# Optimization experiments

Hardware: AMD Instinct MI355X
Metric: run time of the kernel (lower is better)

## Reference

```python
import jax, jax.numpy as jnp
import numpy as np

P = 9    # patch_size (number of shifts per axis)
DP = 1   # dilation_patch (pixel step per shift)


def setup_inputs() -> dict:
    key = jax.random.key(0)
    k1, k2 = jax.random.split(key)
    input1 = jax.random.normal(k1, (4, 256, 96, 128), dtype=jnp.float32)
    input2 = jax.random.normal(k2, (4, 256, 96, 128), dtype=jnp.float32)
    return {"input1": input1, "input2": input2}


def _correlation(input1, input2):
    # Faithful to iter_spatial_correlation_sample with kernel_size=1, stride=1,
    # padding=0, dilation=1: offsets are integer pixel shifts, and bilinear
    # grid_sample (align_corners=True, zeros outside) at integer coordinates is
    # exactly a zero-padded integer shift of input2.
    b, c, h, w = input2.shape
    off = DP * ((P - 1) // 2)  # center offset in pixels
    pad2 = jnp.pad(input2, ((0, 0), (0, 0), (off, off), (off, off)))
    rows = []
    for i in range(P):          # small fixed loop over patch offsets (81 total)
        cols = []
        for j in range(P):
            # window = input2 shifted by (dy, dx) = (i*DP - off, j*DP - off)
            win = jax.lax.dynamic_slice(pad2, (0, 0, i * DP, j * DP), (b, c, h, w))
            cols.append(jnp.einsum('bchw,bchw->bhw', input1, win))
        rows.append(jnp.stack(cols, axis=1))  # [b, P, h, w]
    return jnp.stack(rows, axis=1)            # [b, P, P, h, w]


def reference(input1, input2):
    return _correlation(input1, input2)
```

## Files before the change

### kernel.cpp

```cpp
#include <hip/hip_runtime.h>

#define BB 4
#define CC 256
#define HH 96
#define WW 128
#define PP 9
#define OFF 4
#define CCH 16
#define NPAIR (CCH / 2)
#define NCH (CC / CCH)
#define TPB 288
#define TW 72
#define XCOLS 64

typedef _Float16 h2 __attribute__((ext_vector_type(2)));

__device__ __forceinline__ h2 u2h(unsigned u) { union { unsigned u; h2 h; } x; x.u = u; return x.h; }

#if __has_builtin(__builtin_amdgcn_fdot2)
__device__ __forceinline__ float dot2(h2 a, h2 b, float c) { return __builtin_amdgcn_fdot2(a, b, c, false); }
#else
__device__ __forceinline__ float dot2(h2 a, h2 b, float c) { return c + (float)a[0] * (float)b[0] + (float)a[1] * (float)b[1]; }
#endif

__device__ __forceinline__ unsigned pk(float a, float b) {
#if __has_builtin(__builtin_amdgcn_cvt_pkrtz)
  auto r = __builtin_amdgcn_cvt_pkrtz(a, b);
  unsigned u; __builtin_memcpy(&u, &r, 4); return u;
#else
  h2 h; h[0] = (_Float16)a; h[1] = (_Float16)b;
  unsigned u; __builtin_memcpy(&u, &h, 4); return u;
#endif
}

__global__ __launch_bounds__(TPB, 4) void corr_kernel(const float* __restrict__ in1,
                                                      const float* __restrict__ in2,
                                                      float* __restrict__ out) {
  __shared__ unsigned s2[NPAIR][PP][TW];
  __shared__ unsigned s1[NPAIR][XCOLS];

  const int bx = blockIdx.x;
  const int xcd = bx & 7;
  const int slot = bx >> 3;
  const int xh = slot & 1;
  const int s3 = slot >> 1;
  const int b = s3 / 12;
  const int h = xcd * 12 + (s3 % 12);
  const int xbase = xh * XCOLS;

  const int tid = threadIdx.x;
  const int dy = tid >> 5;
  const int pxg = tid & 31;
  const int L0 = pxg << 1;

  const int sp = tid / 36;
  const int sc2 = tid - sp * 36;
  const int sL = sc2 << 1;
  const int sgx = xbase - OFF + sL;
  const bool colv = (sgx >= 0) && (sgx < WW);
  const int rlo = (h >= OFF) ? 0 : (OFF - h);
  const int rhi = (PP < HH + OFF - h) ? PP : (HH + OFF - h);

  const int plane = HH * WW;
  const long base_b = (long)b * CC * plane;

  const float* p2a = in2 + base_b + (long)(2 * sp) * plane + (long)(h - OFF) * WW + sgx;
  const float* p2b = p2a + plane;
  const int i1p = tid >> 5, i1c = tid & 31;
  const float* p1a = in1 + base_b + (long)(2 * i1p) * plane + h * WW + xbase + (i1c << 1);
  const float* p1b = p1a + plane;

  for (int i = tid; i < NPAIR * PP * TW; i += TPB) ((unsigned*)s2)[i] = 0u;

  float acc[2][PP];
#pragma unroll
  for (int px = 0; px < 2; ++px)
#pragma unroll
    for (int dx = 0; dx < PP; ++dx) acc[px][dx] = 0.f;

  float2 fa[PP], fb[PP], ga, gb;

  if (colv) {
#pragma unroll
    for (int r = 0; r < PP; ++r)
      if (r >= rlo && r < rhi) {
        fa[r] = *(const float2*)(p2a + r * WW);
        fb[r] = *(const float2*)(p2b + r * WW);
      }
  }
  if (tid < NPAIR * 32) { ga = *(const float2*)p1a; gb = *(const float2*)p1b; }
  __syncthreads();

#pragma unroll 1
  for (int c = 0; c < NCH; ++c) {
    if (colv) {
#pragma unroll
      for (int r = 0; r < PP; ++r)
        if (r >= rlo && r < rhi)
          *(uint2*)&s2[sp][r][sL] = make_uint2(pk(fa[r].x, fb[r].x), pk(fa[r].y, fb[r].y));
    }
    if (tid < NPAIR * 32)
      *(uint2*)&s1[i1p][i1c << 1] = make_uint2(pk(ga.x, gb.x), pk(ga.y, gb.y));
    __syncthreads();

    if (c + 1 < NCH) {
      const long adv = (long)(c + 1) * CCH * plane;
      if (colv) {
#pragma unroll
        for (int r = 0; r < PP; ++r)
          if (r >= rlo && r < rhi) {
            fa[r] = *(const float2*)(p2a + adv + r * WW);
            fb[r] = *(const float2*)(p2b + adv + r * WW);
          }
      }
      if (tid < NPAIR * 32) { ga = *(const float2*)(p1a + adv); gb = *(const float2*)(p1b + adv); }
    }

#pragma unroll
    for (int p = 0; p < NPAIR; ++p) {
      unsigned q[2], w[10];
      *(uint2*)q = *(const uint2*)&s1[p][L0];
#pragma unroll
      for (int i = 0; i < 5; ++i)
        *(uint2*)&w[2 * i] = *(const uint2*)&s2[p][dy][L0 + 2 * i];
#pragma unroll
      for (int px = 0; px < 2; ++px)
#pragma unroll
        for (int dx = 0; dx < PP; ++dx)
          acc[px][dx] = dot2(u2h(w[px + dx]), u2h(q[px]), acc[px][dx]);
    }
    __syncthreads();
  }

  const int gx0 = xbase + L0;
  float* ob = out + ((long)(b * PP + dy) * PP) * plane + h * WW + gx0;
#pragma unroll
  for (int dx = 0; dx < PP; ++dx)
    *(float2*)(ob + (long)dx * plane) = make_float2(acc[0][dx], acc[1][dx]);
}

extern "C" void kernel_launch(void* const* d_in, const int* in_sizes, int n_in,
                              void* d_out, int out_size, void* d_ws, size_t ws_size,
                              hipStream_t stream) {
  const float* in1 = (const float*)d_in[0];
  const float* in2 = (const float*)d_in[1];
  float* out = (float*)d_out;
  corr_kernel<<<dim3(BB * HH * 2), dim3(TPB), 0, stream>>>(in1, in2, out);
}
```

Measured before the change: 160.3 us.

## Double-buffer LDS tiles and use one LDS-only barrier per channel chunk

Shared-memory tiles become double-buffered, so the next chunk's fp16-packed data is written into the alternate buffer right after computing on the current one. This removes one of the two barriers per channel chunk. A custom barrier waits only on LDS counters (lgkmcnt) so global prefetches two chunks ahead can stay in flight across it. The cost is twice the LDS footprint, which may lower occupancy, plus more live prefetch registers.

```diff
diff --git a/kernel.cpp b/kernel.cpp
--- a/kernel.cpp
+++ b/kernel.cpp
@@ -33,11 +33,19 @@
 #endif
 }
 
+__device__ __forceinline__ void bar_lgkm() {
+  __builtin_amdgcn_sched_barrier(0);
+  asm volatile("s_waitcnt lgkmcnt(0)" ::: "memory");
+  __builtin_amdgcn_s_barrier();
+  asm volatile("" ::: "memory");
+  __builtin_amdgcn_sched_barrier(0);
+}
+
 __global__ __launch_bounds__(TPB, 4) void corr_kernel(const float* __restrict__ in1,
                                                       const float* __restrict__ in2,
                                                       float* __restrict__ out) {
-  __shared__ unsigned s2[NPAIR][PP][TW];
-  __shared__ unsigned s1[NPAIR][XCOLS];
+  __shared__ unsigned s2[2][NPAIR][PP][TW];
+  __shared__ unsigned s1[2][NPAIR][XCOLS];
 
   const int bx = blockIdx.x;
   const int xcd = bx & 7;
@@ -70,7 +78,7 @@
   const float* p1a = in1 + base_b + (long)(2 * i1p) * plane + h * WW + xbase + (i1c << 1);
   const float* p1b = p1a + plane;
 
-  for (int i = tid; i < NPAIR * PP * TW; i += TPB) ((unsigned*)s2)[i] = 0u;
+  for (int i = tid; i < 2 * NPAIR * PP * TW; i += TPB) ((unsigned*)s2)[i] = 0u;
 
   float acc[2][PP];
 #pragma unroll
@@ -80,56 +88,64 @@
 
   float2 fa[PP], fb[PP], ga, gb;
 
-  if (colv) {
+  auto PREFETCH = [&](int c) {
+    const long adv = (long)c * CCH * plane;
+    if (colv) {
 #pragma unroll
-    for (int r = 0; r < PP; ++r)
-      if (r >= rlo && r < rhi) {
-        fa[r] = *(const float2*)(p2a + r * WW);
-        fb[r] = *(const float2*)(p2b + r * WW);
-      }
-  }
-  if (tid < NPAIR * 32) { ga = *(const float2*)p1a; gb = *(const float2*)p1b; }
-  __syncthreads();
+      for (int r = 0; r < PP; ++r)
+        if (r >= rlo && r < rhi) {
+          fa[r] = *(const float2*)(p2a + adv + r * WW);
+          fb[r] = *(const float2*)(p2b + adv + r * WW);
+        }
+    }
+    if (tid < NPAIR * 32) {
+      ga = *(const float2*)(p1a + adv);
+      gb = *(const float2*)(p1b + adv);
+    }
+  };
 
-#pragma unroll 1
-  for (int c = 0; c < NCH; ++c) {
+  auto STORE = [&](int buf) {
     if (colv) {
 #pragma unroll
       for (int r = 0; r < PP; ++r)
         if (r >= rlo && r < rhi)
-          *(uint2*)&s2[sp][r][sL] = make_uint2(pk(fa[r].x, fb[r].x), pk(fa[r].y, fb[r].y));
+          *(uint2*)&s2[buf][sp][r][sL] = make_uint2(pk(fa[r].x, fb[r].x), pk(fa[r].y, fb[r].y));
     }
     if (tid < NPAIR * 32)
-      *(uint2*)&s1[i1p][i1c << 1] = make_uint2(pk(ga.x, gb.x), pk(ga.y, gb.y));
-    __syncthreads();
+      *(uint2*)&s1[buf][i1p][i1c << 1] = make_uint2(pk(ga.x, gb.x), pk(ga.y, gb.y));
+  };
 
-    if (c + 1 < NCH) {
-      const long adv = (long)(c + 1) * CCH * plane;
-      if (colv) {
-#pragma unroll
-        for (int r = 0; r < PP; ++r)
-          if (r >= rlo && r < rhi) {
-            fa[r] = *(const float2*)(p2a + adv + r * WW);
-            fb[r] = *(const float2*)(p2b + adv + r * WW);
-          }
-      }
-      if (tid < NPAIR * 32) { ga = *(const float2*)(p1a + adv); gb = *(const float2*)(p1b + adv); }
-    }
+  PREFETCH(0);
+  bar_lgkm();
+
+  STORE(0);
+  PREFETCH(1);
+  bar_lgkm();
+
+#pragma unroll 1
+  for (int c = 0; c < NCH; ++c) {
+    const unsigned (*S2)[PP][TW] = s2[c & 1];
+    const unsigned (*S1)[XCOLS] = s1[c & 1];
 
 #pragma unroll
     for (int p = 0; p < NPAIR; ++p) {
       unsigned q[2], w[10];
-      *(uint2*)q = *(const uint2*)&s1[p][L0];
+      *(uint2*)q = *(const uint2*)&S1[p][L0];
 #pragma unroll
       for (int i = 0; i < 5; ++i)
-        *(uint2*)&w[2 * i] = *(const uint2*)&s2[p][dy][L0 + 2 * i];
+        *(uint2*)&w[2 * i] = *(const uint2*)&S2[p][dy][L0 + 2 * i];
 #pragma unroll
       for (int px = 0; px < 2; ++px)
 #pragma unroll
         for (int dx = 0; dx < PP; ++dx)
           acc[px][dx] = dot2(u2h(w[px + dx]), u2h(q[px]), acc[px][dx]);
     }
-    __syncthreads();
+
+    if (c + 1 < NCH) {
+      STORE((c + 1) & 1);
+      if (c + 2 < NCH) PREFETCH(c + 2);
+      bar_lgkm();
+    }
   }
 
   const int gx0 = xbase + L0;
```

Result: slower. 519.0 us (+223.7%).

## Compute correlation with MFMA 16x16x32 f16 tiles over 3-row bands

Applied to the files above, without the earlier changes.

Replaces the per-thread fdot2 accumulation with MFMA matrix instructions. Each block handles a 3-row by 32-pixel tile and computes a 32x32 pixel-pair Gram block per dy, then extracts the 9 diagonals through shared memory. The staging and tiling are restructured around this: channels are packed in chunks of 32, the in2 rows are shared across three output rows, and the grid is reshaped to 512 blocks. About two thirds of the MFMA work is off-diagonal and gets discarded. The epilogue adds extra syncs and strided scalar stores, and the register prefetch of the next chunk is dropped.

```diff
diff --git a/kernel.cpp b/kernel.cpp
--- a/kernel.cpp
+++ b/kernel.cpp
@@ -6,137 +6,142 @@
 #define WW 128
 #define PP 9
 #define OFF 4
-#define CCH 16
-#define NPAIR (CCH / 2)
-#define NCH (CC / CCH)
-#define TPB 288
-#define TW 72
-#define XCOLS 64
+#define PLANE (HH * WW)
 
-typedef _Float16 h2 __attribute__((ext_vector_type(2)));
+#define HB 3
+#define RN (HB + 8)
+#define PX 32
+#define SW 48
+#define PAD 20
+#define KCH 32
+#define NCHK (CC / KCH)
+#define TPB 384
+#define DPAD 36
 
-__device__ __forceinline__ h2 u2h(unsigned u) { union { unsigned u; h2 h; } x; x.u = u; return x.h; }
+typedef _Float16 f16x8 __attribute__((ext_vector_type(8)));
+typedef float fx4 __attribute__((ext_vector_type(4)));
 
-#if __has_builtin(__builtin_amdgcn_fdot2)
-__device__ __forceinline__ float dot2(h2 a, h2 b, float c) { return __builtin_amdgcn_fdot2(a, b, c, false); }
-#else
-__device__ __forceinline__ float dot2(h2 a, h2 b, float c) { return c + (float)a[0] * (float)b[0] + (float)a[1] * (float)b[1]; }
-#endif
+union U16 { uint4 u; f16x8 h; };
 
 __device__ __forceinline__ unsigned pk(float a, float b) {
 #if __has_builtin(__builtin_amdgcn_cvt_pkrtz)
   auto r = __builtin_amdgcn_cvt_pkrtz(a, b);
   unsigned u; __builtin_memcpy(&u, &r, 4); return u;
 #else
-  h2 h; h[0] = (_Float16)a; h[1] = (_Float16)b;
-  unsigned u; __builtin_memcpy(&u, &h, 4); return u;
+  _Float16 h0 = (_Float16)a, h1 = (_Float16)b;
+  unsigned u = 0; __builtin_memcpy(&u, &h0, 2); unsigned v = 0; __builtin_memcpy(&v, &h1, 2);
+  return u | (v << 16);
 #endif
 }
 
-__global__ __launch_bounds__(TPB, 4) void corr_kernel(const float* __restrict__ in1,
+__global__ __launch_bounds__(TPB, 3) void corr_kernel(const float* __restrict__ in1,
                                                       const float* __restrict__ in2,
                                                       float* __restrict__ out) {
-  __shared__ unsigned s2[NPAIR][PP][TW];
-  __shared__ unsigned s1[NPAIR][XCOLS];
+  __shared__ __align__(16) unsigned s2[RN][SW][PAD];
+  __shared__ __align__(16) unsigned s1[HB][PX][PAD];
 
   const int bx = blockIdx.x;
   const int xcd = bx & 7;
-  const int slot = bx >> 3;
-  const int xh = slot & 1;
-  const int s3 = slot >> 1;
-  const int b = s3 / 12;
-  const int h = xcd * 12 + (s3 % 12);
-  const int xbase = xh * XCOLS;
+  const int s = bx >> 3;
+  const int xq = s & 3;
+  const int t2 = s >> 2;
+  const int b = t2 & 3;
+  const int band = xcd * 4 + (t2 >> 2);
+  const int h0 = band * HB;
 
   const int tid = threadIdx.x;
-  const int dy = tid >> 5;
-  const int pxg = tid & 31;
-  const int L0 = pxg << 1;
+  const int wv = tid >> 6;
+  const int wr = wv >> 1;
+  const int wp = wv & 1;
+  const int lane = tid & 63;
+  const int ln = lane & 15;
+  const int lg = lane >> 4;
 
-  const int sp = tid / 36;
-  const int sc2 = tid - sp * 36;
-  const int sL = sc2 << 1;
-  const int sgx = xbase - OFF + sL;
-  const bool colv = (sgx >= 0) && (sgx < WW);
-  const int rlo = (h >= OFF) ? 0 : (OFF - h);
-  const int rhi = (PP < HH + OFF - h) ? PP : (HH + OFF - h);
+  const int spx = tid % 48;
+  const int sq = tid / 48;
+  const int scb = sq & 3;
+  const int sr0 = sq >> 2;
+  const int gx2 = xq * PX - OFF + spx;
+  const bool okx = (unsigned)gx2 < WW;
+  const int tpx = tid & 31;
+  const int tq = tid >> 5;
+  const int tcb = tq & 3;
+  const int tr = tq >> 2;
 
-  const int plane = HH * WW;
-  const long base_b = (long)b * CC * plane;
+  const long cpl = (long)PLANE;
+  const float* b2 = in2 + ((long)b * CC + scb * 8) * cpl + gx2;
+  const float* b1 = in1 + ((long)b * CC + tcb * 8) * cpl + (long)(h0 + tr) * WW + xq * PX + tpx;
 
-  const float* p2a = in2 + base_b + (long)(2 * sp) * plane + (long)(h - OFF) * WW + sgx;
-  const float* p2b = p2a + plane;
-  const int i1p = tid >> 5, i1c = tid & 31;
-  const float* p1a = in1 + base_b + (long)(2 * i1p) * plane + h * WW + xbase + (i1c << 1);
-  const float* p1b = p1a + plane;
-
-  for (int i = tid; i < NPAIR * PP * TW; i += TPB) ((unsigned*)s2)[i] = 0u;
-
-  float acc[2][PP];
-#pragma unroll
-  for (int px = 0; px < 2; ++px)
-#pragma unroll
-    for (int dx = 0; dx < PP; ++dx) acc[px][dx] = 0.f;
-
-  float2 fa[PP], fb[PP], ga, gb;
-
-  if (colv) {
-#pragma unroll
-    for (int r = 0; r < PP; ++r)
-      if (r >= rlo && r < rhi) {
-        fa[r] = *(const float2*)(p2a + r * WW);
-        fb[r] = *(const float2*)(p2b + r * WW);
-      }
-  }
-  if (tid < NPAIR * 32) { ga = *(const float2*)p1a; gb = *(const float2*)p1b; }
+  for (int i = tid; i < RN * SW * PAD; i += TPB) ((unsigned*)s2)[i] = 0u;
   __syncthreads();
 
+  fx4 acc[PP][2];
+#pragma unroll
+  for (int dy = 0; dy < PP; ++dy)
+#pragma unroll
+    for (int t = 0; t < 2; ++t) acc[dy][t] = (fx4)0.f;
+
 #pragma unroll 1
-  for (int c = 0; c < NCH; ++c) {
-    if (colv) {
+  for (int c = 0; c < NCHK; ++c) {
+    const long cadv = (long)c * KCH * cpl;
 #pragma unroll
-      for (int r = 0; r < PP; ++r)
-        if (r >= rlo && r < rhi)
-          *(uint2*)&s2[sp][r][sL] = make_uint2(pk(fa[r].x, fb[r].x), pk(fa[r].y, fb[r].y));
+    for (int k = 0; k < 6; ++k) {
+      const int r = sr0 + 2 * k;
+      const int rg = h0 - OFF + r;
+      if (r < RN && okx && (unsigned)rg < HH) {
+        const float* p = b2 + cadv + (long)rg * WW;
+        const float l0 = p[0], l1 = p[cpl], l2 = p[2 * cpl], l3 = p[3 * cpl];
+        const float l4 = p[4 * cpl], l5 = p[5 * cpl], l6 = p[6 * cpl], l7 = p[7 * cpl];
+        uint4 w;
+        w.x = pk(l0, l1); w.y = pk(l2, l3); w.z = pk(l4, l5); w.w = pk(l6, l7);
+        *(uint4*)&s2[r][spx][4 * scb] = w;
+      }
     }
-    if (tid < NPAIR * 32)
-      *(uint2*)&s1[i1p][i1c << 1] = make_uint2(pk(ga.x, gb.x), pk(ga.y, gb.y));
+    {
+      const float* p = b1 + cadv;
+      const float l0 = p[0], l1 = p[cpl], l2 = p[2 * cpl], l3 = p[3 * cpl];
+      const float l4 = p[4 * cpl], l5 = p[5 * cpl], l6 = p[6 * cpl], l7 = p[7 * cpl];
+      uint4 w;
+      w.x = pk(l0, l1); w.y = pk(l2, l3); w.z = pk(l4, l5); w.w = pk(l6, l7);
+      *(uint4*)&s1[tr][tpx][4 * tcb] = w;
+    }
     __syncthreads();
 
-    if (c + 1 < NCH) {
-      const long adv = (long)(c + 1) * CCH * plane;
-      if (colv) {
+    U16 a; a.u = *(const uint4*)&s1[wr][wp * 16 + ln][4 * lg];
 #pragma unroll
-        for (int r = 0; r < PP; ++r)
-          if (r >= rlo && r < rhi) {
-            fa[r] = *(const float2*)(p2a + adv + r * WW);
-            fb[r] = *(const float2*)(p2b + adv + r * WW);
-          }
+    for (int dy = 0; dy < PP; ++dy) {
+#pragma unroll
+      for (int t = 0; t < 2; ++t) {
+        U16 bb; bb.u = *(const uint4*)&s2[wr + dy][wp * 16 + 16 * t + ln][4 * lg];
+        acc[dy][t] = __builtin_amdgcn_mfma_f32_16x16x32_f16(a.h, bb.h, acc[dy][t], 0, 0, 0);
       }
-      if (tid < NPAIR * 32) { ga = *(const float2*)(p1a + adv); gb = *(const float2*)(p1b + adv); }
-    }
-
-#pragma unroll
-    for (int p = 0; p < NPAIR; ++p) {
-      unsigned q[2], w[10];
-      *(uint2*)q = *(const uint2*)&s1[p][L0];
-#pragma unroll
-      for (int i = 0; i < 5; ++i)
-        *(uint2*)&w[2 * i] = *(const uint2*)&s2[p][dy][L0 + 2 * i];
-#pragma unroll
-      for (int px = 0; px < 2; ++px)
-#pragma unroll
-        for (int dx = 0; dx < PP; ++dx)
-          acc[px][dx] = dot2(u2h(w[px + dx]), u2h(q[px]), acc[px][dx]);
     }
     __syncthreads();
   }
 
-  const int gx0 = xbase + L0;
-  float* ob = out + ((long)(b * PP + dy) * PP) * plane + h * WW + gx0;
+  float* DL = (float*)&s2[0][0][0];
 #pragma unroll
-  for (int dx = 0; dx < PP; ++dx)
-    *(float2*)(ob + (long)dx * plane) = make_float2(acc[0][dx], acc[1][dx]);
+  for (int dy = 0; dy < PP; ++dy) {
+#pragma unroll
+    for (int t = 0; t < 2; ++t) {
+      const int p2 = wp * 16 + 16 * t + ln;
+      *(fx4*)&DL[(wr * SW + p2) * DPAD + wp * 16 + 4 * lg] = acc[dy][t];
+    }
+    __syncthreads();
+#pragma unroll
+    for (int k = 0; k < 3; ++k) {
+      const int id = tid + TPB * k;
+      if (id < HB * PP * PX) {
+        const int px = id & 31;
+        const int v = id >> 5;
+        const int dx = v % PP;
+        const int rr = v / PP;
+        const float val = DL[(rr * SW + px + dx) * DPAD + px];
+        out[(long)((b * PP + dy) * PP + dx) * PLANE + (long)(h0 + rr) * WW + xq * PX + px] = val;
+      }
+    }
+    __syncthreads();
+  }
 }
 
 extern "C" void kernel_launch(void* const* d_in, const int* in_sizes, int n_in,
@@ -145,5 +150,5 @@
   const float* in1 = (const float*)d_in[0];
   const float* in2 = (const float*)d_in[1];
   float* out = (float*)d_out;
-  corr_kernel<<<dim3(BB * HH * 2), dim3(TPB), 0, stream>>>(in1, in2, out);
+  corr_kernel<<<dim3(512), dim3(TPB), 0, stream>>>(in1, in2, out);
 }
```

Result: faster. 145.5 us (-9.3%).
